# Kernel optimization log

Hardware: AMD Instinct MI355X
Metric: run time of the kernel (lower is better)

Reference implementation:

```python
import jax, jax.numpy as jnp
import numpy as np

DEPTH, B, S, E, H, EXP = 6, 16, 511, 1024, 16, 2
HD = E // H
FF = EXP * E


def _layernorm(x, g, b, eps=1e-5):
    m = jnp.mean(x, axis=-1, keepdims=True)
    v = jnp.var(x, axis=-1, keepdims=True)
    return (x - m) * jax.lax.rsqrt(v + eps) * g + b


def setup_inputs() -> dict:
    key = jax.random.key(0)
    ks = jax.random.split(key, 12)
    sc = 0.02
    inp = {
        "x": jax.random.normal(ks[0], (B, S, E), jnp.float32),
        "cls_token": jax.random.normal(ks[1], (1, 1, E), jnp.float32),
        "pos_emb": jax.random.normal(ks[2], (1, S + 1, E), jnp.float32),
        # attention projections (bias=False in source), stacked over depth
        "Wq": jax.random.normal(ks[3], (DEPTH, E, E), jnp.float32) * sc,
        "Wk": jax.random.normal(ks[4], (DEPTH, E, E), jnp.float32) * sc,
        "Wv": jax.random.normal(ks[5], (DEPTH, E, E), jnp.float32) * sc,
        "Wp": jax.random.normal(ks[6], (DEPTH, E, E), jnp.float32) * sc,
        # layernorm params
        "ln1_g": jnp.ones((DEPTH, E), jnp.float32),
        "ln1_b": jnp.zeros((DEPTH, E), jnp.float32),
        "ln2_g": jnp.ones((DEPTH, E), jnp.float32),
        "ln2_b": jnp.zeros((DEPTH, E), jnp.float32),
        # feed-forward (with bias, as nn.Linear default)
        "W1": jax.random.normal(ks[7], (DEPTH, E, FF), jnp.float32) * sc,
        "b1": jnp.zeros((DEPTH, FF), jnp.float32),
        "W2": jax.random.normal(ks[8], (DEPTH, FF, E), jnp.float32) * sc,
        "b2": jnp.zeros((DEPTH, E), jnp.float32),
    }
    return inp


def reference(x, cls_token, pos_emb, Wq, Wk, Wv, Wp,
              ln1_g, ln1_b, ln2_g, ln2_b, W1, b1, W2, b2):
    b = x.shape[0]
    # AddClsToken + PositionalEmbedding
    h = jnp.concatenate([jnp.broadcast_to(cls_token, (b, 1, E)), x], axis=1) + pos_emb
    scale = jnp.asarray(E ** 0.5, h.dtype)  # source scales by sqrt(emb_size)
    for i in range(DEPTH):
        # --- self-attention sublayer (pre-LN) ---
        res = h
        xn = _layernorm(h, ln1_g[i], ln1_b[i])
        q = (xn @ Wq[i]).reshape(b, -1, H, HD).transpose(0, 2, 1, 3)  # b h n d
        k = (xn @ Wk[i]).reshape(b, -1, H, HD).transpose(0, 2, 1, 3)
        v = (xn @ Wv[i]).reshape(b, -1, H, HD).transpose(0, 2, 1, 3)
        energy = jnp.einsum('bhqd,bhkd->bhqk', q, k)
        att = jax.nn.softmax(energy / scale, axis=-1)
        out = jnp.einsum('bhqk,bhkd->bhqd', att, v)
        out = out.transpose(0, 2, 1, 3).reshape(b, -1, E)
        h = out @ Wp[i] + res
        # --- feed-forward sublayer (pre-LN) ---
        res = h
        yn = _layernorm(h, ln2_g[i], ln2_b[i])
        ff = jax.nn.gelu(yn @ W1[i] + b1[i], approximate=False) @ W2[i] + b2[i]
        h = ff + res
    return h
```

## Files before the change

### kernel.cpp

```cpp
#include <hip/hip_runtime.h>
#include <cstdint>
#include <cstddef>

#define DEPTH 6
#define NB    16
#define NSEQ  512
#define EMB   1024
#define NHEAD 16
#define HDIM  64
#define FFD   2048
#define NTOK  (NB * NSEQ)

typedef unsigned short u16;
using bf16x8 = __attribute__((ext_vector_type(8))) __bf16;
using f32x4  = __attribute__((ext_vector_type(4))) float;
using f32x16 = __attribute__((ext_vector_type(16))) float;
using u16x4  = __attribute__((ext_vector_type(4))) u16;
using u16x8  = __attribute__((ext_vector_type(8))) u16;

typedef __attribute__((address_space(1))) uint32_t* as1_u32p;
typedef __attribute__((address_space(3))) uint32_t* as3_u32p;

__device__ __forceinline__ u16 f2bf(float f) {
  union { float f; uint32_t u; } v; v.f = f;
  uint32_t u = v.u;
  return (u16)((u + 0x7FFFu + ((u >> 16) & 1u)) >> 16);
}

__device__ __forceinline__ void gload_lds16(const u16* g, u16* l) {
  void* gp = const_cast<u16*>(g);
  __builtin_amdgcn_global_load_lds((as1_u32p)gp, (as3_u32p)l, 16, 0, 0);
}

template<int ROWBYTES>
__device__ __forceinline__ void stage16k(const u16* g0, int ldk, u16* lds) {
  int t = threadIdx.x;
#pragma unroll
  for (int i = 0; i < 4; ++i) {
    int off = (i * 256 + t) * 16;
    int row = off / ROWBYTES;
    int pc  = (off % ROWBYTES) >> 4;
    int lc  = pc ^ (row & 7);
    gload_lds16(g0 + (size_t)row * ldk + lc * 8, lds + (off >> 1));
  }
}

__global__ __launch_bounds__(256)
void wprep_k(const float* __restrict__ W, u16* __restrict__ Wt,
             int K, int N, size_t inL, size_t outL, size_t outOff)
{
  int ntiles = N >> 6, ktiles = K >> 6;
  int bid = blockIdx.x;
  int l = bid / (ktiles * ntiles);
  int r = bid % (ktiles * ntiles);
  int kt = r / ntiles, nt = r % ntiles;
  const float* in = W + (size_t)l * inL + (size_t)(kt * 64) * N + nt * 64;
  u16* out = Wt + (size_t)l * outL + outOff + (size_t)(nt * 64) * K + kt * 64;
  __shared__ float tile[64][65];
  int t = threadIdx.x;
  int tr = t >> 4, tc = (t & 15) * 4;
#pragma unroll
  for (int i = 0; i < 4; ++i) {
    f32x4 v = *(const f32x4*)(in + (size_t)(tr + i * 16) * N + tc);
    tile[tr + i * 16][tc + 0] = v[0];
    tile[tr + i * 16][tc + 1] = v[1];
    tile[tr + i * 16][tc + 2] = v[2];
    tile[tr + i * 16][tc + 3] = v[3];
  }
  __syncthreads();
#pragma unroll
  for (int i = 0; i < 4; ++i) {
    int nr = tr + i * 16;
    u16x4 o;
    o[0] = f2bf(tile[tc + 0][nr]);
    o[1] = f2bf(tile[tc + 1][nr]);
    o[2] = f2bf(tile[tc + 2][nr]);
    o[3] = f2bf(tile[tc + 3][nr]);
    *(u16x4*)(out + (size_t)nr * K + tc) = o;
  }
}

__global__ __launch_bounds__(256)
void embed_k(const float* __restrict__ x, const float* __restrict__ cls,
             const float* __restrict__ pos, float* __restrict__ H)
{
  int row = blockIdx.x, t = threadIdx.x;
  int b_ = row >> 9, n = row & 511;
  int c = t * 4;
  f32x4 p = *(const f32x4*)(pos + (size_t)n * EMB + c);
  f32x4 s;
  if (n == 0) s = *(const f32x4*)(cls + c);
  else        s = *(const f32x4*)(x + ((size_t)b_ * 511 + (n - 1)) * EMB + c);
  f32x4 o = s + p;
  *(f32x4*)(H + (size_t)row * EMB + c) = o;
}

__global__ __launch_bounds__(256)
void ln_k(const float* __restrict__ H, const float* __restrict__ g,
          const float* __restrict__ b, u16* __restrict__ out)
{
  int row = blockIdx.x, t = threadIdx.x;
  const float* hp = H + (size_t)row * EMB;
  f32x4 v = *(const f32x4*)(hp + t * 4);
  float s  = v[0] + v[1] + v[2] + v[3];
  float ss = v[0]*v[0] + v[1]*v[1] + v[2]*v[2] + v[3]*v[3];
#pragma unroll
  for (int m = 1; m <= 32; m <<= 1) { s += __shfl_xor(s, m); ss += __shfl_xor(ss, m); }
  __shared__ float red[8];
  if ((t & 63) == 0) { red[(t >> 6) * 2] = s; red[(t >> 6) * 2 + 1] = ss; }
  __syncthreads();
  float S  = red[0] + red[2] + red[4] + red[6];
  float SS = red[1] + red[3] + red[5] + red[7];
  float mean = S * (1.0f / EMB);
  float var  = SS * (1.0f / EMB) - mean * mean;
  float rs = rsqrtf(var + 1e-5f);
  f32x4 gg = *(const f32x4*)(g + t * 4);
  f32x4 bb = *(const f32x4*)(b + t * 4);
  u16x4 o;
#pragma unroll
  for (int i = 0; i < 4; ++i) o[i] = f2bf((v[i] - mean) * rs * gg[i] + bb[i]);
  *(u16x4*)(out + (size_t)row * EMB + t * 4) = o;
}

template<int EPI>
__global__ __launch_bounds__(256, 3)
void gemm_k(const u16* __restrict__ A, const u16* __restrict__ Bt,
            int nbn, int K,
            const float* __restrict__ bias, float* __restrict__ H,
            u16* __restrict__ outB,
            u16* __restrict__ qo, u16* __restrict__ ko, u16* __restrict__ vto)
{
  __shared__ u16 sm[16384];
  int cpx = gridDim.x >> 3;
  int logical = (blockIdx.x & 7) * cpx + (blockIdx.x >> 3);
  int bm = logical / nbn, bn = logical % nbn;
  int t = threadIdx.x, lane = t & 63, w = t >> 6;
  int wm = w >> 1, wn = w & 1;
  const u16* Ab = A  + (size_t)(bm * 128) * K;
  const u16* Bb = Bt + (size_t)(bn * 128) * K;
  int nkt = K >> 6;

  const f32x4 vzero = {0.f, 0.f, 0.f, 0.f};
  f32x4 acc[4][4];
#pragma unroll
  for (int i = 0; i < 4; ++i)
#pragma unroll
    for (int j = 0; j < 4; ++j) acc[i][j] = vzero;

  int r0 = lane & 15;
  int hi = lane >> 4;
  int kk0 = hi * 8;

  for (int kt = 0; kt < nkt; ++kt) {
    stage16k<128>(Ab + kt * 64, K, sm);
    stage16k<128>(Bb + kt * 64, K, sm + 8192);
    __syncthreads();
    const char* smAp = (const char*)sm;
    const char* smBp = (const char*)(sm + 8192);
#pragma unroll
    for (int ks = 0; ks < 2; ++ks) {
      int kk = ks * 32 + kk0;
      bf16x8 a[4], b[4];
#pragma unroll
      for (int mf = 0; mf < 4; ++mf) {
        int row = wm * 64 + mf * 16 + r0;
        a[mf] = *(const bf16x8*)(smAp + row * 128 + ((kk * 2) ^ ((row & 7) << 4)));
      }
#pragma unroll
      for (int nf = 0; nf < 4; ++nf) {
        int row = wn * 64 + nf * 16 + r0;
        b[nf] = *(const bf16x8*)(smBp + row * 128 + ((kk * 2) ^ ((row & 7) << 4)));
      }
#pragma unroll
      for (int mf = 0; mf < 4; ++mf)
#pragma unroll
        for (int nf = 0; nf < 4; ++nf)
          acc[mf][nf] = __builtin_amdgcn_mfma_f32_16x16x32_bf16(a[mf], b[nf], acc[mf][nf], 0, 0, 0);
    }
    __syncthreads();
  }

  if (EPI == 1 || EPI == 3) {
    int m0 = bm * 128 + wm * 64;
    int n0 = bn * 128 + wn * 64;
#pragma unroll
    for (int mf = 0; mf < 4; ++mf) {
#pragma unroll
      for (int nf = 0; nf < 4; ++nf) {
        int col  = n0 + nf * 16 + r0;
        int rowb = m0 + mf * 16 + hi * 4;
#pragma unroll
        for (int j = 0; j < 4; ++j) {
          float v = acc[mf][nf][j];
          size_t idx = (size_t)(rowb + j) * EMB + col;
          if (EPI == 1) H[idx] = v + H[idx];
          else          H[idx] = v + bias[col] + H[idx];
        }
      }
    }
    return;
  }

  int sec = (bn * 128) >> 10;
  bool vsec = (EPI == 0) && (sec == 2);
#pragma unroll
  for (int mf = 0; mf < 4; ++mf) {
#pragma unroll
    for (int nf = 0; nf < 4; ++nf) {
      int colL = wn * 64 + nf * 16 + r0;
#pragma unroll
      for (int j = 0; j < 4; ++j) {
        int rowL = wm * 64 + mf * 16 + hi * 4 + j;
        float v = acc[mf][nf][j];
        if (EPI == 2) {
          float xg = v + bias[bn * 128 + colL];
          v = 0.5f * xg * (1.0f + erff(xg * 0.70710678118654752f));
        }
        u16 o = f2bf(v);
        if (!vsec)
          sm[rowL * 128 + (colL & 7) + ((((colL >> 3) ^ (rowL & 7))) << 3)] = o;
        else
          sm[colL * 128 + (rowL & 7) + ((((rowL >> 3) ^ (colL & 7))) << 3)] = o;
      }
    }
  }
  __syncthreads();

  int c  = t & 15;
  int rb = t >> 4;
  if (!vsec) {
#pragma unroll
    for (int i = 0; i < 8; ++i) {
      int row = rb * 8 + i;
      u16x8 v = *(const u16x8*)(sm + row * 128 + ((c ^ (row & 7)) << 3));
      if (EPI == 2) {
        int rowg = bm * 128 + row;
        int colg = bn * 128 + c * 8;
        *(u16x8*)(outB + (size_t)rowg * FFD + colg) = v;
      } else {
        int n_ = bm * 128 + row;
        int b_ = n_ >> 9, tok = n_ & 511;
        int c0 = (bn * 128 - sec * 1024) + c * 8;
        int hh = c0 >> 6, d0 = c0 & 63;
        u16* dst = (sec == 0) ? qo : ko;
        *(u16x8*)(dst + (((size_t)(b_ * NHEAD + hh) * NSEQ + tok) * HDIM) + d0) = v;
      }
    }
  } else {
#pragma unroll
    for (int i = 0; i < 8; ++i) {
      int rowp = rb * 8 + i;
      u16x8 v = *(const u16x8*)(sm + rowp * 128 + ((c ^ (rowp & 7)) << 3));
      int c0 = (bn * 128 - 2048) + rowp;
      int hh = c0 >> 6, d = c0 & 63;
      int tok0 = bm * 128 + c * 8;
      int b_ = tok0 >> 9;
      *(u16x8*)(vto + ((size_t)(b_ * NHEAD + hh) * HDIM + d) * NSEQ + (tok0 & 511)) = v;
    }
  }
}

__global__ __launch_bounds__(256, 2)
void attn_k(const u16* __restrict__ Q, const u16* __restrict__ Kk,
            const u16* __restrict__ Vt, u16* __restrict__ AO)
{
  __shared__ u16 bufK[2][8192];
  __shared__ u16 bufV[2][8192];
  int bid = blockIdx.x;
  int logical = (bid & 7) * 128 + (bid >> 3);
  int bh = logical >> 2, qt = logical & 3;
  int t = threadIdx.x, lane = t & 63, w = t >> 6;
  int l31 = lane & 31, hi32 = lane >> 5;
  const u16* Kb = Kk + (size_t)bh * (NSEQ * HDIM);
  const u16* Vb = Vt + (size_t)bh * (HDIM * NSEQ);

  int qbase = qt * 128 + w * 32;
  const u16* Qp = Q + ((size_t)bh * NSEQ + qbase + l31) * HDIM;
  bf16x8 qf[4];
#pragma unroll
  for (int tk = 0; tk < 4; ++tk)
    qf[tk] = *(const bf16x8*)(Qp + 16 * tk + 8 * hi32);

  stage16k<128>(Kb, HDIM, &bufK[0][0]);
  stage16k<256>(Vb, NSEQ, &bufV[0][0]);
  __syncthreads();

  f32x16 accO[2];
#pragma unroll
  for (int r = 0; r < 16; ++r) { accO[0][r] = 0.f; accO[1][r] = 0.f; }
  float m_run = -1e30f, den = 0.f;
  const float inv32 = 0.03125f;

  for (int c = 0; c < 4; ++c) {
    if (c < 3) {
      stage16k<128>(Kb + (size_t)(c + 1) * 128 * HDIM, HDIM, &bufK[(c + 1) & 1][0]);
      stage16k<256>(Vb + (c + 1) * 128, NSEQ, &bufV[(c + 1) & 1][0]);
    }
    const char* smK = (const char*)&bufK[c & 1][0];
    f32x16 s[4];
#pragma unroll
    for (int kt = 0; kt < 4; ++kt) {
#pragma unroll
      for (int r = 0; r < 16; ++r) s[kt][r] = 0.f;
#pragma unroll
      for (int tk = 0; tk < 4; ++tk) {
        int row = kt * 32 + l31;
        bf16x8 kf = *(const bf16x8*)(smK + row * 128 +
                      ((32 * tk + 16 * hi32) ^ ((row & 7) << 4)));
        s[kt] = __builtin_amdgcn_mfma_f32_32x32x16_bf16(kf, qf[tk], s[kt], 0, 0, 0);
      }
    }
    float mc = -1e30f;
#pragma unroll
    for (int kt = 0; kt < 4; ++kt)
#pragma unroll
      for (int r = 0; r < 16; ++r) mc = fmaxf(mc, s[kt][r]);
    mc = fmaxf(mc, __shfl_xor(mc, 32));
    float newm = fmaxf(m_run, mc);
    float fac = __expf((m_run - newm) * inv32);
    den *= fac;
#pragma unroll
    for (int r = 0; r < 16; ++r) { accO[0][r] *= fac; accO[1][r] *= fac; }
    m_run = newm;
#pragma unroll
    for (int kt = 0; kt < 4; ++kt)
#pragma unroll
      for (int r = 0; r < 16; ++r) {
        float p = __expf((s[kt][r] - newm) * inv32);
        den += p;
        s[kt][r] = p;
      }
    uint32_t pb[32];
#pragma unroll
    for (int j = 0; j < 32; ++j) {
      float lo = s[j >> 3][(2 * j) & 15];
      float hi = s[j >> 3][((2 * j) & 15) + 1];
      asm("v_cvt_pk_bf16_f32 %0, %1, %2" : "=v"(pb[j]) : "v"(lo), "v"(hi));
    }
    const char* smV = (const char*)&bufV[c & 1][0];
#pragma unroll
    for (int ks = 0; ks < 8; ++ks) {
      uint32_t x0 = pb[4 * ks], y0 = pb[4 * ks + 2];
      uint32_t x1 = pb[4 * ks + 1], y1 = pb[4 * ks + 3];
      asm("v_permlane32_swap_b32 %0, %1" : "+v"(x0), "+v"(y0));
      asm("v_permlane32_swap_b32 %0, %1" : "+v"(x1), "+v"(y1));
      union { uint4 u; bf16x8 v; } pa;
      pa.u = make_uint4(x0, x1, y0, y1);
#pragma unroll
      for (int dt = 0; dt < 2; ++dt) {
        int row = dt * 32 + l31;
        bf16x8 vb = *(const bf16x8*)(smV + row * 256 +
                      ((32 * ks + 16 * hi32) ^ ((row & 7) << 4)));
        accO[dt] = __builtin_amdgcn_mfma_f32_32x32x16_bf16(pa.v, vb, accO[dt], 0, 0, 0);
      }
    }
    __syncthreads();
  }

  float denf = den + __shfl_xor(den, 32);
  float rden = 1.0f / denf;
  int b_ = bh >> 4, hh = bh & 15;
#pragma unroll
  for (int r = 0; r < 16; ++r) {
    int qoff = (r & 3) + 8 * (r >> 2) + 4 * hi32;
    float rd = __shfl(rden, qoff);
    int tok = qbase + qoff;
    size_t base = ((size_t)(b_ * NSEQ + tok)) * EMB + hh * 64 + l31;
    AO[base]      = f2bf(accO[0][r] * rd);
    AO[base + 32] = f2bf(accO[1][r] * rd);
  }
}

extern "C" void kernel_launch(void* const* d_in, const int* in_sizes, int n_in,
                              void* d_out, int out_size, void* d_ws, size_t ws_size,
                              hipStream_t stream)
{
  const float* x    = (const float*)d_in[0];
  const float* cls  = (const float*)d_in[1];
  const float* pos  = (const float*)d_in[2];
  const float* Wq   = (const float*)d_in[3];
  const float* Wk   = (const float*)d_in[4];
  const float* Wv   = (const float*)d_in[5];
  const float* Wp   = (const float*)d_in[6];
  const float* ln1g = (const float*)d_in[7];
  const float* ln1b = (const float*)d_in[8];
  const float* ln2g = (const float*)d_in[9];
  const float* ln2b = (const float*)d_in[10];
  const float* W1   = (const float*)d_in[11];
  const float* b1   = (const float*)d_in[12];
  const float* W2   = (const float*)d_in[13];
  const float* b2   = (const float*)d_in[14];
  float* H = (float*)d_out;

  char* ws = (char*)d_ws;
  u16* wqkv = (u16*)(ws + 0);
  u16* wp   = (u16*)(ws + 37748736);
  u16* w1t  = (u16*)(ws + 50331648);
  u16* w2t  = (u16*)(ws + 75497472);
  u16* xn   = (u16*)(ws + 100663296);
  u16* qb   = (u16*)(ws + 117440512);
  u16* kb   = (u16*)(ws + 134217728);
  u16* vtb  = (u16*)(ws + 150994944);
  u16* ffb  = qb;

  wprep_k<<<1536, 256, 0, stream>>>(Wq, wqkv, 1024, 1024, 1048576, 3145728, 0);
  wprep_k<<<1536, 256, 0, stream>>>(Wk, wqkv, 1024, 1024, 1048576, 3145728, 1048576);
  wprep_k<<<1536, 256, 0, stream>>>(Wv, wqkv, 1024, 1024, 1048576, 3145728, 2097152);
  wprep_k<<<1536, 256, 0, stream>>>(Wp, wp,   1024, 1024, 1048576, 1048576, 0);
  wprep_k<<<3072, 256, 0, stream>>>(W1, w1t,  1024, 2048, 2097152, 2097152, 0);
  wprep_k<<<3072, 256, 0, stream>>>(W2, w2t,  2048, 1024, 2097152, 2097152, 0);

  embed_k<<<NTOK, 256, 0, stream>>>(x, cls, pos, H);

  for (int l = 0; l < DEPTH; ++l) {
    ln_k<<<NTOK, 256, 0, stream>>>(H, ln1g + l * EMB, ln1b + l * EMB, xn);
    gemm_k<0><<<64 * 24, 256, 0, stream>>>(xn, wqkv + (size_t)l * 3145728, 24, 1024,
                                           nullptr, nullptr, nullptr, qb, kb, vtb);
    attn_k<<<1024, 256, 0, stream>>>(qb, kb, vtb, xn);
    gemm_k<1><<<64 * 8, 256, 0, stream>>>(xn, wp + (size_t)l * 1048576, 8, 1024,
                                          nullptr, H, nullptr, nullptr, nullptr, nullptr);
    ln_k<<<NTOK, 256, 0, stream>>>(H, ln2g + l * EMB, ln2b + l * EMB, xn);
    gemm_k<2><<<64 * 16, 256, 0, stream>>>(xn, w1t + (size_t)l * 2097152, 16, 1024,
                                           b1 + l * FFD, nullptr, ffb, nullptr, nullptr, nullptr);
    gemm_k<3><<<64 * 8, 256, 0, stream>>>(ffb, w2t + (size_t)l * 2097152, 8, 2048,
                                          b2 + l * EMB, H, nullptr, nullptr, nullptr, nullptr);
  }
}
```

Baseline: 1.453 ms.

## Double-buffer GEMM shared-memory tiles and use one wavefront per LayerNorm row

The GEMM kernel now keeps two LDS tile buffers, prefetches two K-tiles ahead, and waits with explicit vmcnt and s_barrier, so global-to-LDS loads overlap the MFMA work instead of stalling behind a full sync each iteration. Doubling LDS use drops the occupancy hint from 3 to 2 blocks per CU. LayerNorm is also changed to process four rows per block, one wavefront per row, which removes the shared-memory reduction and the block barrier. The vmcnt(8) wait assumes a fixed count of outstanding loads per stage from stage16k, and an incorrect count could cause a race.

```diff
diff --git a/kernel.cpp b/kernel.cpp
--- a/kernel.cpp
+++ b/kernel.cpp
@@ -99,38 +99,42 @@
 void ln_k(const float* __restrict__ H, const float* __restrict__ g,
           const float* __restrict__ b, u16* __restrict__ out)
 {
-  int row = blockIdx.x, t = threadIdx.x;
+  int lane = threadIdx.x & 63, w = threadIdx.x >> 6;
+  int row = blockIdx.x * 4 + w;
   const float* hp = H + (size_t)row * EMB;
-  f32x4 v = *(const f32x4*)(hp + t * 4);
-  float s  = v[0] + v[1] + v[2] + v[3];
-  float ss = v[0]*v[0] + v[1]*v[1] + v[2]*v[2] + v[3]*v[3];
+  f32x4 v[4];
+  float s = 0.f, ss = 0.f;
+#pragma unroll
+  for (int i = 0; i < 4; ++i) {
+    v[i] = *(const f32x4*)(hp + lane * 4 + i * 256);
+#pragma unroll
+    for (int j = 0; j < 4; ++j) { s += v[i][j]; ss += v[i][j] * v[i][j]; }
+  }
 #pragma unroll
   for (int m = 1; m <= 32; m <<= 1) { s += __shfl_xor(s, m); ss += __shfl_xor(ss, m); }
-  __shared__ float red[8];
-  if ((t & 63) == 0) { red[(t >> 6) * 2] = s; red[(t >> 6) * 2 + 1] = ss; }
-  __syncthreads();
-  float S  = red[0] + red[2] + red[4] + red[6];
-  float SS = red[1] + red[3] + red[5] + red[7];
-  float mean = S * (1.0f / EMB);
-  float var  = SS * (1.0f / EMB) - mean * mean;
+  float mean = s * (1.0f / EMB);
+  float var  = ss * (1.0f / EMB) - mean * mean;
   float rs = rsqrtf(var + 1e-5f);
-  f32x4 gg = *(const f32x4*)(g + t * 4);
-  f32x4 bb = *(const f32x4*)(b + t * 4);
-  u16x4 o;
-#pragma unroll
-  for (int i = 0; i < 4; ++i) o[i] = f2bf((v[i] - mean) * rs * gg[i] + bb[i]);
-  *(u16x4*)(out + (size_t)row * EMB + t * 4) = o;
+#pragma unroll
+  for (int i = 0; i < 4; ++i) {
+    f32x4 gg = *(const f32x4*)(g + lane * 4 + i * 256);
+    f32x4 bb = *(const f32x4*)(b + lane * 4 + i * 256);
+    u16x4 o;
+#pragma unroll
+    for (int j = 0; j < 4; ++j) o[j] = f2bf((v[i][j] - mean) * rs * gg[j] + bb[j]);
+    *(u16x4*)(out + (size_t)row * EMB + lane * 4 + i * 256) = o;
+  }
 }
 
 template<int EPI>
-__global__ __launch_bounds__(256, 3)
+__global__ __launch_bounds__(256, 2)
 void gemm_k(const u16* __restrict__ A, const u16* __restrict__ Bt,
             int nbn, int K,
             const float* __restrict__ bias, float* __restrict__ H,
             u16* __restrict__ outB,
             u16* __restrict__ qo, u16* __restrict__ ko, u16* __restrict__ vto)
 {
-  __shared__ u16 sm[16384];
+  __shared__ u16 sm[2][16384];
   int cpx = gridDim.x >> 3;
   int logical = (blockIdx.x & 7) * cpx + (blockIdx.x >> 3);
   int bm = logical / nbn, bn = logical % nbn;
@@ -151,12 +155,17 @@
   int hi = lane >> 4;
   int kk0 = hi * 8;
 
+  stage16k<128>(Ab, K, &sm[0][0]);
+  stage16k<128>(Bb, K, &sm[0][8192]);
+  stage16k<128>(Ab + 64, K, &sm[1][0]);
+  stage16k<128>(Bb + 64, K, &sm[1][8192]);
+
   for (int kt = 0; kt < nkt; ++kt) {
-    stage16k<128>(Ab + kt * 64, K, sm);
-    stage16k<128>(Bb + kt * 64, K, sm + 8192);
-    __syncthreads();
-    const char* smAp = (const char*)sm;
-    const char* smBp = (const char*)(sm + 8192);
+    if (kt == nkt - 1) asm volatile("s_waitcnt vmcnt(0)" ::: "memory");
+    else               asm volatile("s_waitcnt vmcnt(8)" ::: "memory");
+    asm volatile("s_barrier" ::: "memory");
+    const char* smAp = (const char*)&sm[kt & 1][0];
+    const char* smBp = (const char*)&sm[kt & 1][8192];
 #pragma unroll
     for (int ks = 0; ks < 2; ++ks) {
       int kk = ks * 32 + kk0;
@@ -177,7 +186,11 @@
         for (int nf = 0; nf < 4; ++nf)
           acc[mf][nf] = __builtin_amdgcn_mfma_f32_16x16x32_bf16(a[mf], b[nf], acc[mf][nf], 0, 0, 0);
     }
-    __syncthreads();
+    asm volatile("s_barrier" ::: "memory");
+    if (kt + 2 < nkt) {
+      stage16k<128>(Ab + (kt + 2) * 64, K, &sm[kt & 1][0]);
+      stage16k<128>(Bb + (kt + 2) * 64, K, &sm[kt & 1][8192]);
+    }
   }
 
   if (EPI == 1 || EPI == 3) {
@@ -201,6 +214,7 @@
     return;
   }
 
+  u16* smE = &sm[0][0];
   int sec = (bn * 128) >> 10;
   bool vsec = (EPI == 0) && (sec == 2);
 #pragma unroll
@@ -218,9 +232,9 @@
         }
         u16 o = f2bf(v);
         if (!vsec)
-          sm[rowL * 128 + (colL & 7) + ((((colL >> 3) ^ (rowL & 7))) << 3)] = o;
+          smE[rowL * 128 + (colL & 7) + ((((colL >> 3) ^ (rowL & 7))) << 3)] = o;
         else
-          sm[colL * 128 + (rowL & 7) + ((((rowL >> 3) ^ (colL & 7))) << 3)] = o;
+          smE[colL * 128 + (rowL & 7) + ((((rowL >> 3) ^ (colL & 7))) << 3)] = o;
       }
     }
   }
@@ -232,7 +246,7 @@
 #pragma unroll
     for (int i = 0; i < 8; ++i) {
       int row = rb * 8 + i;
-      u16x8 v = *(const u16x8*)(sm + row * 128 + ((c ^ (row & 7)) << 3));
+      u16x8 v = *(const u16x8*)(smE + row * 128 + ((c ^ (row & 7)) << 3));
       if (EPI == 2) {
         int rowg = bm * 128 + row;
         int colg = bn * 128 + c * 8;
@@ -250,7 +264,7 @@
 #pragma unroll
     for (int i = 0; i < 8; ++i) {
       int rowp = rb * 8 + i;
-      u16x8 v = *(const u16x8*)(sm + rowp * 128 + ((c ^ (rowp & 7)) << 3));
+      u16x8 v = *(const u16x8*)(smE + rowp * 128 + ((c ^ (rowp & 7)) << 3));
       int c0 = (bn * 128 - 2048) + rowp;
       int hh = c0 >> 6, d = c0 & 63;
       int tok0 = bm * 128 + c * 8;
@@ -413,13 +427,13 @@
   embed_k<<<NTOK, 256, 0, stream>>>(x, cls, pos, H);
 
   for (int l = 0; l < DEPTH; ++l) {
-    ln_k<<<NTOK, 256, 0, stream>>>(H, ln1g + l * EMB, ln1b + l * EMB, xn);
+    ln_k<<<2048, 256, 0, stream>>>(H, ln1g + l * EMB, ln1b + l * EMB, xn);
     gemm_k<0><<<64 * 24, 256, 0, stream>>>(xn, wqkv + (size_t)l * 3145728, 24, 1024,
                                            nullptr, nullptr, nullptr, qb, kb, vtb);
     attn_k<<<1024, 256, 0, stream>>>(qb, kb, vtb, xn);
     gemm_k<1><<<64 * 8, 256, 0, stream>>>(xn, wp + (size_t)l * 1048576, 8, 1024,
                                           nullptr, H, nullptr, nullptr, nullptr, nullptr);
-    ln_k<<<NTOK, 256, 0, stream>>>(H, ln2g + l * EMB, ln2b + l * EMB, xn);
+    ln_k<<<2048, 256, 0, stream>>>(H, ln2g + l * EMB, ln2b + l * EMB, xn);
     gemm_k<2><<<64 * 16, 256, 0, stream>>>(xn, w1t + (size_t)l * 2097152, 16, 1024,
                                            b1 + l * FFD, nullptr, ffb, nullptr, nullptr, nullptr);
     gemm_k<3><<<64 * 8, 256, 0, stream>>>(ffb, w2t + (size_t)l * 2097152, 8, 2048,
```

New measurement: 1.461 ms. No clear change (+0.5%).
